# Optimization experiments

Measured on AMD Instinct MI355X. Metric: run time of the kernel, lower is better.

The kernel has to match this reference:

```python
import jax, jax.numpy as jnp
import numpy as np

BLOCK_SIZE = 64
WINDOW_SIZE = 256  # local_window pattern: each query block attends to blocks within the window
NEG_INF = -1e30


def setup_inputs() -> dict:
    key = jax.random.key(0)
    kq, kk, kv = jax.random.split(key, 3)
    B, S, H, D = 2, 4096, 16, 64
    q = jax.random.normal(kq, (B, S, H, D), dtype=jnp.float32)
    k = jax.random.normal(kk, (B, S, H, D), dtype=jnp.float32)
    v = jax.random.normal(kv, (B, S, H, D), dtype=jnp.float32)
    return {"q": q, "k": k, "v": v}


def _block_sparse_attn(q, k, v):
    # q, k, v: [B, S, H, D]
    B, S, H, D = q.shape
    bs = BLOCK_SIZE
    N = S // bs                      # number of blocks
    W = WINDOW_SIZE // bs            # window in blocks (4)
    half = W // 2
    offsets = jnp.arange(-half, half + 1)          # [K] neighbor offsets, K = W+1 = 5
    K = offsets.shape[0]

    i = jnp.arange(N)
    j = i[:, None] + offsets[None, :]              # [N, K] neighbor block ids
    valid = (j >= 0) & (j < N)                     # boundary mask
    jc = jnp.clip(j, 0, N - 1)

    # reshape into blocks: [B, H, N, bs, D]
    qb = q.reshape(B, N, bs, H, D).transpose(0, 3, 1, 2, 4)
    kb = k.reshape(B, N, bs, H, D).transpose(0, 3, 1, 2, 4)
    vb = v.reshape(B, N, bs, H, D).transpose(0, 3, 1, 2, 4)

    # gather only the active (neighbor) key/value blocks: [B, H, N, K, bs, D]
    kn = kb[:, :, jc]
    vn = vb[:, :, jc]

    scale = 1.0 / jnp.sqrt(jnp.asarray(D, dtype=q.dtype))
    # block scores: [B, H, N, bs, K, bs]
    scores = jnp.einsum('bhnqd,bhnkcd->bhnqkc', qb, kn) * scale
    scores = jnp.where(valid[None, None, :, None, :, None], scores, NEG_INF)

    # softmax over the union of active key blocks for each query block
    scores = scores.reshape(B, H, N, bs, K * bs)
    attn = jax.nn.softmax(scores, axis=-1)
    out = jnp.einsum('bhnqe,bhned->bhnqd', attn, vn.reshape(B, H, N, K * bs, D))

    # back to [B, S, H, D]
    return out.transpose(0, 2, 3, 1, 4).reshape(B, S, H, D)


def reference(q, k, v):
    return _block_sparse_attn(q, k, v)
```

## Files before the change

kernel.cpp:

```cpp
#include <hip/hip_runtime.h>

#define S_DIM 4096
#define H_DIM 16
#define D_DIM 64
#define N_BLK 64
#define NEG_INF_F (-1e30f)
#define QSCALE 0.125f

typedef __attribute__((ext_vector_type(4))) float f32x4;
typedef __attribute__((ext_vector_type(8))) short s16x8;
typedef __attribute__((ext_vector_type(4))) unsigned int u32x4;
typedef __attribute__((ext_vector_type(2))) unsigned int u32x2;

__device__ __forceinline__ unsigned int fbits(float f) {
    return __builtin_bit_cast(unsigned int, f);
}
__device__ __forceinline__ unsigned int pkbf(float a, float b) {
    return __builtin_amdgcn_perm(fbits(b) + 0x8000u, fbits(a) + 0x8000u, 0x07060302u);
}

__global__ __launch_bounds__(256, 2) void bsattn_kernel(
    const float* __restrict__ qg, const float* __restrict__ kg,
    const float* __restrict__ vg, float* __restrict__ outg)
{
    __shared__ unsigned int lds_vt[D_DIM * 256];

    const int tid  = threadIdx.x;
    const int w    = tid >> 6;
    const int lane = tid & 63;
    const int quad = lane >> 4;
    const int l16  = lane & 15;

    const int b  = blockIdx.z;
    const int h  = blockIdx.y;
    const int n0 = blockIdx.x << 2;
    const int n  = n0 + w;

    s16x8 bq[4][2];
#pragma unroll
    for (int qt = 0; qt < 4; ++qt) {
        const size_t qrow = ((size_t)(b * S_DIM + n * 64 + qt * 16 + l16) * H_DIM + h) * D_DIM;
#pragma unroll
        for (int hh = 0; hh < 2; ++hh) {
            const float4* qp = reinterpret_cast<const float4*>(qg + qrow + hh * 32 + quad * 8);
            float4 f0 = qp[0];
            float4 f1 = qp[1];
            u32x4 u;
            u.x = pkbf(f0.x * QSCALE, f0.y * QSCALE);
            u.y = pkbf(f0.z * QSCALE, f0.w * QSCALE);
            u.z = pkbf(f1.x * QSCALE, f1.y * QSCALE);
            u.w = pkbf(f1.z * QSCALE, f1.w * QSCALE);
            bq[qt][hh] = __builtin_bit_cast(s16x8, u);
        }
    }

    {
        const int jt = tid >> 5;
        const int sp = tid & 31;
        const int jv = n0 - 2 + jt;
        if (jv >= 0 && jv < N_BLK) {
            const float* v0p = vg + ((size_t)(b * S_DIM + jv * 64 + 2 * sp) * H_DIM + h) * D_DIM;
            const float* v1p = v0p + H_DIM * D_DIM;
            const int craw = jt * 64 + 2 * sp;
#pragma unroll
            for (int ch = 0; ch < 4; ++ch) {
                const int d0 = ch * 16;
                const float4* ap = reinterpret_cast<const float4*>(v0p + d0);
                const float4* bp = reinterpret_cast<const float4*>(v1p + d0);
                float4 a0 = ap[0], a1 = ap[1], a2 = ap[2], a3 = ap[3];
                float4 b0 = bp[0], b1 = bp[1], b2 = bp[2], b3 = bp[3];
                float av[16] = {a0.x,a0.y,a0.z,a0.w, a1.x,a1.y,a1.z,a1.w,
                                a2.x,a2.y,a2.z,a2.w, a3.x,a3.y,a3.z,a3.w};
                float bv[16] = {b0.x,b0.y,b0.z,b0.w, b1.x,b1.y,b1.z,b1.w,
                                b2.x,b2.y,b2.z,b2.w, b3.x,b3.y,b3.z,b3.w};
#pragma unroll
                for (int i = 0; i < 16; ++i) {
                    const int d = d0 + i;
                    lds_vt[d * 256 + (((craw + 8 * d) & 511) >> 1)] = pkbf(av[i], bv[i]);
                }
            }
        }
    }

    f32x4 o[4][4];
    float m_run[4], l_run[4];
#pragma unroll
    for (int qt = 0; qt < 4; ++qt) {
        m_run[qt] = NEG_INF_F; l_run[qt] = 0.f;
#pragma unroll
        for (int dt = 0; dt < 4; ++dt) o[qt][dt] = (f32x4){0.f, 0.f, 0.f, 0.f};
    }

    __syncthreads();

    const int colb = quad * 4 + 8 * l16;

    for (int t = 0; t < 5; ++t) {
        const int j = n - 2 + t;
        if (j < 0 || j >= N_BLK) continue;
        const int ji = w + t;

        float4 kf[4][2][2];
#pragma unroll
        for (int kt = 0; kt < 4; ++kt) {
            const size_t krow = ((size_t)(b * S_DIM + j * 64 + kt * 16 + l16) * H_DIM + h) * D_DIM + quad * 8;
#pragma unroll
            for (int hh = 0; hh < 2; ++hh) {
                const float4* kp = reinterpret_cast<const float4*>(kg + krow + hh * 32);
                kf[kt][hh][0] = kp[0];
                kf[kt][hh][1] = kp[1];
            }
        }
        s16x8 kbf[4][2];
#pragma unroll
        for (int kt = 0; kt < 4; ++kt)
#pragma unroll
            for (int hh = 0; hh < 2; ++hh) {
                u32x4 u;
                u.x = pkbf(kf[kt][hh][0].x, kf[kt][hh][0].y);
                u.y = pkbf(kf[kt][hh][0].z, kf[kt][hh][0].w);
                u.z = pkbf(kf[kt][hh][1].x, kf[kt][hh][1].y);
                u.w = pkbf(kf[kt][hh][1].z, kf[kt][hh][1].w);
                kbf[kt][hh] = __builtin_bit_cast(s16x8, u);
            }

        s16x8 pa[4][2];
#pragma unroll
        for (int qt = 0; qt < 4; ++qt) {
            f32x4 sa[4];
#pragma unroll
            for (int kt = 0; kt < 4; ++kt) {
                f32x4 z = {0.f, 0.f, 0.f, 0.f};
                f32x4 a0 = __builtin_amdgcn_mfma_f32_16x16x32_bf16(kbf[kt][0], bq[qt][0], z, 0, 0, 0);
                sa[kt]   = __builtin_amdgcn_mfma_f32_16x16x32_bf16(kbf[kt][1], bq[qt][1], a0, 0, 0, 0);
            }
            float mx = NEG_INF_F;
#pragma unroll
            for (int kt = 0; kt < 4; ++kt)
#pragma unroll
                for (int r = 0; r < 4; ++r) mx = fmaxf(mx, sa[kt][r]);
            mx = fmaxf(mx, __shfl_xor(mx, 16));
            mx = fmaxf(mx, __shfl_xor(mx, 32));
            const float mn = fmaxf(m_run[qt], mx);
            const float alpha = __expf(m_run[qt] - mn);
            m_run[qt] = mn;

            float rs = 0.f;
            unsigned int pk[4][2];
#pragma unroll
            for (int kt = 0; kt < 4; ++kt) {
                float e0 = __expf(sa[kt][0] - mn);
                float e1 = __expf(sa[kt][1] - mn);
                float e2 = __expf(sa[kt][2] - mn);
                float e3 = __expf(sa[kt][3] - mn);
                rs += (e0 + e1) + (e2 + e3);
                pk[kt][0] = pkbf(e0, e1);
                pk[kt][1] = pkbf(e2, e3);
            }
            rs += __shfl_xor(rs, 16);
            rs += __shfl_xor(rs, 32);
            l_run[qt] = l_run[qt] * alpha + rs;

            float ab[4];
#pragma unroll
            for (int r = 0; r < 4; ++r)
                ab[r] = __shfl(alpha, (lane & 48) + quad * 4 + r);
#pragma unroll
            for (int dt = 0; dt < 4; ++dt)
#pragma unroll
                for (int r = 0; r < 4; ++r) o[qt][dt][r] *= ab[r];

            pa[qt][0] = __builtin_bit_cast(s16x8, (u32x4){pk[0][0], pk[0][1], pk[1][0], pk[1][1]});
            pa[qt][1] = __builtin_bit_cast(s16x8, (u32x4){pk[2][0], pk[2][1], pk[3][0], pk[3][1]});
        }

        const int cb0 = ji * 64 + colb;
#pragma unroll
        for (int dt = 0; dt < 4; ++dt) {
            const int d = dt * 16 + l16;
            const unsigned int* vrow = lds_vt + d * 256;
            const int cb = cb0 + 128 * dt;
            u32x2 v00 = *reinterpret_cast<const u32x2*>(vrow + (((cb     ) & 511) >> 1));
            u32x2 v01 = *reinterpret_cast<const u32x2*>(vrow + (((cb + 16) & 511) >> 1));
            u32x2 v10 = *reinterpret_cast<const u32x2*>(vrow + (((cb + 32) & 511) >> 1));
            u32x2 v11 = *reinterpret_cast<const u32x2*>(vrow + (((cb + 48) & 511) >> 1));
            s16x8 vf0 = __builtin_bit_cast(s16x8, (u32x4){v00.x, v00.y, v01.x, v01.y});
            s16x8 vf1 = __builtin_bit_cast(s16x8, (u32x4){v10.x, v10.y, v11.x, v11.y});
#pragma unroll
            for (int qt = 0; qt < 4; ++qt) {
                o[qt][dt] = __builtin_amdgcn_mfma_f32_16x16x32_bf16(pa[qt][0], vf0, o[qt][dt], 0, 0, 0);
                o[qt][dt] = __builtin_amdgcn_mfma_f32_16x16x32_bf16(pa[qt][1], vf1, o[qt][dt], 0, 0, 0);
            }
        }
    }

#pragma unroll
    for (int qt = 0; qt < 4; ++qt) {
#pragma unroll
        for (int r = 0; r < 4; ++r) {
            const float lb = __shfl(l_run[qt], (lane & 48) + quad * 4 + r);
            const float inv = 1.0f / lb;
            const int row = n * 64 + qt * 16 + quad * 4 + r;
            float* op = outg + ((size_t)(b * S_DIM + row) * H_DIM + h) * D_DIM + l16;
#pragma unroll
            for (int dt = 0; dt < 4; ++dt)
                op[dt * 16] = o[qt][dt][r] * inv;
        }
    }
}

extern "C" void kernel_launch(void* const* d_in, const int* in_sizes, int n_in,
                              void* d_out, int out_size, void* d_ws, size_t ws_size,
                              hipStream_t stream) {
    const float* q = (const float*)d_in[0];
    const float* k = (const float*)d_in[1];
    const float* v = (const float*)d_in[2];
    float* out = (float*)d_out;
    const int B = in_sizes[0] / (S_DIM * H_DIM * D_DIM);
    dim3 grid(N_BLK / 4, H_DIM, B);
    dim3 block(256);
    hipLaunchKernelGGL(bsattn_kernel, grid, block, 0, stream, q, k, v, out);
}
```

Measured before the change: 159.7 us.

## Software-pipeline K block loads with double-buffered registers across window tiles

Unrolls the five-tile window loop and prefetches the next K block into a second register buffer while the current tile's QK, softmax and PV MFMAs run. Clamped block indices keep the loads in bounds, and boundary tiles skip only the compute. This targets global-load latency that was exposed at the start of each tile. The extra registers lead to lowering launch bounds from two blocks per CU to one, which can reduce occupancy and latency hiding across waves.

After: 173.3 us. +8.5%, slower.

```diff
diff --git a/kernel.cpp b/kernel.cpp
--- a/kernel.cpp
+++ b/kernel.cpp
@@ -19,7 +19,109 @@
     return __builtin_amdgcn_perm(fbits(b) + 0x8000u, fbits(a) + 0x8000u, 0x07060302u);
 }
 
-__global__ __launch_bounds__(256, 2) void bsattn_kernel(
+__device__ __forceinline__ void load_k(const float* __restrict__ kb, float4 (&kf)[4][2][2]) {
+#pragma unroll
+    for (int kt = 0; kt < 4; ++kt) {
+        const float4* kp = reinterpret_cast<const float4*>(kb + (size_t)kt * (16 * H_DIM * D_DIM));
+#pragma unroll
+        for (int hh = 0; hh < 2; ++hh) {
+            kf[kt][hh][0] = kp[hh * 8 + 0];
+            kf[kt][hh][1] = kp[hh * 8 + 1];
+        }
+    }
+}
+
+__device__ __forceinline__ void conv_k(const float4 (&kf)[4][2][2], s16x8 (&kbf)[4][2]) {
+#pragma unroll
+    for (int kt = 0; kt < 4; ++kt)
+#pragma unroll
+        for (int hh = 0; hh < 2; ++hh) {
+            u32x4 u;
+            u.x = pkbf(kf[kt][hh][0].x, kf[kt][hh][0].y);
+            u.y = pkbf(kf[kt][hh][0].z, kf[kt][hh][0].w);
+            u.z = pkbf(kf[kt][hh][1].x, kf[kt][hh][1].y);
+            u.w = pkbf(kf[kt][hh][1].z, kf[kt][hh][1].w);
+            kbf[kt][hh] = __builtin_bit_cast(s16x8, u);
+        }
+}
+
+__device__ __forceinline__ void compute_tile(
+    const s16x8 (&kbf)[4][2], const s16x8 (&bq)[4][2],
+    f32x4 (&o)[4][4], float (&m_run)[4], float (&l_run)[4],
+    const unsigned int* __restrict__ lds_vt, int cb0, int lane, int quad)
+{
+    s16x8 pa[4][2];
+#pragma unroll
+    for (int qt = 0; qt < 4; ++qt) {
+        f32x4 sa[4];
+#pragma unroll
+        for (int kt = 0; kt < 4; ++kt) {
+            f32x4 z = {0.f, 0.f, 0.f, 0.f};
+            f32x4 a0 = __builtin_amdgcn_mfma_f32_16x16x32_bf16(kbf[kt][0], bq[qt][0], z, 0, 0, 0);
+            sa[kt]   = __builtin_amdgcn_mfma_f32_16x16x32_bf16(kbf[kt][1], bq[qt][1], a0, 0, 0, 0);
+        }
+        const float ma = fmaxf(fmaxf(sa[0][0], sa[0][1]), fmaxf(sa[0][2], sa[0][3]));
+        const float mb = fmaxf(fmaxf(sa[1][0], sa[1][1]), fmaxf(sa[1][2], sa[1][3]));
+        const float mc = fmaxf(fmaxf(sa[2][0], sa[2][1]), fmaxf(sa[2][2], sa[2][3]));
+        const float md = fmaxf(fmaxf(sa[3][0], sa[3][1]), fmaxf(sa[3][2], sa[3][3]));
+        float mx = fmaxf(fmaxf(ma, mb), fmaxf(mc, md));
+        mx = fmaxf(mx, __shfl_xor(mx, 16));
+        mx = fmaxf(mx, __shfl_xor(mx, 32));
+        const float mn = fmaxf(m_run[qt], mx);
+        const float alpha = __expf(m_run[qt] - mn);
+        m_run[qt] = mn;
+
+        float rsk[4];
+        unsigned int pk[4][2];
+#pragma unroll
+        for (int kt = 0; kt < 4; ++kt) {
+            float e0 = __expf(sa[kt][0] - mn);
+            float e1 = __expf(sa[kt][1] - mn);
+            float e2 = __expf(sa[kt][2] - mn);
+            float e3 = __expf(sa[kt][3] - mn);
+            rsk[kt] = (e0 + e1) + (e2 + e3);
+            pk[kt][0] = pkbf(e0, e1);
+            pk[kt][1] = pkbf(e2, e3);
+        }
+        float rs = (rsk[0] + rsk[1]) + (rsk[2] + rsk[3]);
+        rs += __shfl_xor(rs, 16);
+        rs += __shfl_xor(rs, 32);
+        l_run[qt] = l_run[qt] * alpha + rs;
+
+        float ab[4];
+#pragma unroll
+        for (int r = 0; r < 4; ++r)
+            ab[r] = __shfl(alpha, (lane & 48) + quad * 4 + r);
+#pragma unroll
+        for (int dt = 0; dt < 4; ++dt)
+#pragma unroll
+            for (int r = 0; r < 4; ++r) o[qt][dt][r] *= ab[r];
+
+        pa[qt][0] = __builtin_bit_cast(s16x8, (u32x4){pk[0][0], pk[0][1], pk[1][0], pk[1][1]});
+        pa[qt][1] = __builtin_bit_cast(s16x8, (u32x4){pk[2][0], pk[2][1], pk[3][0], pk[3][1]});
+    }
+
+    const int l16 = lane & 15;
+#pragma unroll
+    for (int dt = 0; dt < 4; ++dt) {
+        const int d = dt * 16 + l16;
+        const unsigned int* vrow = lds_vt + d * 256;
+        const int cb = cb0 + 128 * dt;
+        u32x2 v00 = *reinterpret_cast<const u32x2*>(vrow + (((cb     ) & 511) >> 1));
+        u32x2 v01 = *reinterpret_cast<const u32x2*>(vrow + (((cb + 16) & 511) >> 1));
+        u32x2 v10 = *reinterpret_cast<const u32x2*>(vrow + (((cb + 32) & 511) >> 1));
+        u32x2 v11 = *reinterpret_cast<const u32x2*>(vrow + (((cb + 48) & 511) >> 1));
+        s16x8 vf0 = __builtin_bit_cast(s16x8, (u32x4){v00.x, v00.y, v01.x, v01.y});
+        s16x8 vf1 = __builtin_bit_cast(s16x8, (u32x4){v10.x, v10.y, v11.x, v11.y});
+#pragma unroll
+        for (int qt = 0; qt < 4; ++qt) {
+            o[qt][dt] = __builtin_amdgcn_mfma_f32_16x16x32_bf16(pa[qt][0], vf0, o[qt][dt], 0, 0, 0);
+            o[qt][dt] = __builtin_amdgcn_mfma_f32_16x16x32_bf16(pa[qt][1], vf1, o[qt][dt], 0, 0, 0);
+        }
+    }
+}
+
+__global__ __launch_bounds__(256, 1) void bsattn_kernel(
     const float* __restrict__ qg, const float* __restrict__ kg,
     const float* __restrict__ vg, float* __restrict__ outg)
 {
@@ -35,6 +137,14 @@
     const int h  = blockIdx.y;
     const int n0 = blockIdx.x << 2;
     const int n  = n0 + w;
+
+    const float* kbase = kg + ((size_t)(b * S_DIM) * H_DIM + h) * D_DIM + ((size_t)l16 * H_DIM) * D_DIM + quad * 8;
+#define KPTR(jj) (kbase + (size_t)(jj) * (64 * H_DIM * D_DIM))
+#define JCLAMP(jj) ((jj) < 0 ? 0 : ((jj) > (N_BLK - 1) ? (N_BLK - 1) : (jj)))
+
+    float4 kfA[4][2][2], kfB[4][2][2];
+    s16x8 kbf[4][2];
+    load_k(KPTR(JCLAMP(n - 2)), kfA);
 
     s16x8 bq[4][2];
 #pragma unroll
@@ -95,104 +205,32 @@
 
     const int colb = quad * 4 + 8 * l16;
 
-    for (int t = 0; t < 5; ++t) {
-        const int j = n - 2 + t;
-        if (j < 0 || j >= N_BLK) continue;
-        const int ji = w + t;
-
-        float4 kf[4][2][2];
-#pragma unroll
-        for (int kt = 0; kt < 4; ++kt) {
-            const size_t krow = ((size_t)(b * S_DIM + j * 64 + kt * 16 + l16) * H_DIM + h) * D_DIM + quad * 8;
-#pragma unroll
-            for (int hh = 0; hh < 2; ++hh) {
-                const float4* kp = reinterpret_cast<const float4*>(kg + krow + hh * 32);
-                kf[kt][hh][0] = kp[0];
-                kf[kt][hh][1] = kp[1];
-            }
-        }
-        s16x8 kbf[4][2];
-#pragma unroll
-        for (int kt = 0; kt < 4; ++kt)
-#pragma unroll
-            for (int hh = 0; hh < 2; ++hh) {
-                u32x4 u;
-                u.x = pkbf(kf[kt][hh][0].x, kf[kt][hh][0].y);
-                u.y = pkbf(kf[kt][hh][0].z, kf[kt][hh][0].w);
-                u.z = pkbf(kf[kt][hh][1].x, kf[kt][hh][1].y);
-                u.w = pkbf(kf[kt][hh][1].z, kf[kt][hh][1].w);
-                kbf[kt][hh] = __builtin_bit_cast(s16x8, u);
-            }
-
-        s16x8 pa[4][2];
-#pragma unroll
-        for (int qt = 0; qt < 4; ++qt) {
-            f32x4 sa[4];
-#pragma unroll
-            for (int kt = 0; kt < 4; ++kt) {
-                f32x4 z = {0.f, 0.f, 0.f, 0.f};
-                f32x4 a0 = __builtin_amdgcn_mfma_f32_16x16x32_bf16(kbf[kt][0], bq[qt][0], z, 0, 0, 0);
-                sa[kt]   = __builtin_amdgcn_mfma_f32_16x16x32_bf16(kbf[kt][1], bq[qt][1], a0, 0, 0, 0);
-            }
-            float mx = NEG_INF_F;
-#pragma unroll
-            for (int kt = 0; kt < 4; ++kt)
-#pragma unroll
-                for (int r = 0; r < 4; ++r) mx = fmaxf(mx, sa[kt][r]);
-            mx = fmaxf(mx, __shfl_xor(mx, 16));
-            mx = fmaxf(mx, __shfl_xor(mx, 32));
-            const float mn = fmaxf(m_run[qt], mx);
-            const float alpha = __expf(m_run[qt] - mn);
-            m_run[qt] = mn;
-
-            float rs = 0.f;
-            unsigned int pk[4][2];
-#pragma unroll
-            for (int kt = 0; kt < 4; ++kt) {
-                float e0 = __expf(sa[kt][0] - mn);
-                float e1 = __expf(sa[kt][1] - mn);
-                float e2 = __expf(sa[kt][2] - mn);
-                float e3 = __expf(sa[kt][3] - mn);
-                rs += (e0 + e1) + (e2 + e3);
-                pk[kt][0] = pkbf(e0, e1);
-                pk[kt][1] = pkbf(e2, e3);
-            }
-            rs += __shfl_xor(rs, 16);
-            rs += __shfl_xor(rs, 32);
-            l_run[qt] = l_run[qt] * alpha + rs;
-
-            float ab[4];
-#pragma unroll
-            for (int r = 0; r < 4; ++r)
-                ab[r] = __shfl(alpha, (lane & 48) + quad * 4 + r);
-#pragma unroll
-            for (int dt = 0; dt < 4; ++dt)
-#pragma unroll
-                for (int r = 0; r < 4; ++r) o[qt][dt][r] *= ab[r];
-
-            pa[qt][0] = __builtin_bit_cast(s16x8, (u32x4){pk[0][0], pk[0][1], pk[1][0], pk[1][1]});
-            pa[qt][1] = __builtin_bit_cast(s16x8, (u32x4){pk[2][0], pk[2][1], pk[3][0], pk[3][1]});
-        }
-
-        const int cb0 = ji * 64 + colb;
-#pragma unroll
-        for (int dt = 0; dt < 4; ++dt) {
-            const int d = dt * 16 + l16;
-            const unsigned int* vrow = lds_vt + d * 256;
-            const int cb = cb0 + 128 * dt;
-            u32x2 v00 = *reinterpret_cast<const u32x2*>(vrow + (((cb     ) & 511) >> 1));
-            u32x2 v01 = *reinterpret_cast<const u32x2*>(vrow + (((cb + 16) & 511) >> 1));
-            u32x2 v10 = *reinterpret_cast<const u32x2*>(vrow + (((cb + 32) & 511) >> 1));
-            u32x2 v11 = *reinterpret_cast<const u32x2*>(vrow + (((cb + 48) & 511) >> 1));
-            s16x8 vf0 = __builtin_bit_cast(s16x8, (u32x4){v00.x, v00.y, v01.x, v01.y});
-            s16x8 vf1 = __builtin_bit_cast(s16x8, (u32x4){v10.x, v10.y, v11.x, v11.y});
-#pragma unroll
-            for (int qt = 0; qt < 4; ++qt) {
-                o[qt][dt] = __builtin_amdgcn_mfma_f32_16x16x32_bf16(pa[qt][0], vf0, o[qt][dt], 0, 0, 0);
-                o[qt][dt] = __builtin_amdgcn_mfma_f32_16x16x32_bf16(pa[qt][1], vf1, o[qt][dt], 0, 0, 0);
-            }
-        }
-    }
+    conv_k(kfA, kbf);
+
+    load_k(KPTR(JCLAMP(n - 1)), kfB);
+    if (n - 2 >= 0)
+        compute_tile(kbf, bq, o, m_run, l_run, lds_vt, (w + 0) * 64 + colb, lane, quad);
+    conv_k(kfB, kbf);
+
+    load_k(KPTR(JCLAMP(n)), kfA);
+    if (n - 1 >= 0)
+        compute_tile(kbf, bq, o, m_run, l_run, lds_vt, (w + 1) * 64 + colb, lane, quad);
+    conv_k(kfA, kbf);
+
+    load_k(KPTR(JCLAMP(n + 1)), kfB);
+    compute_tile(kbf, bq, o, m_run, l_run, lds_vt, (w + 2) * 64 + colb, lane, quad);
+    conv_k(kfB, kbf);
+
+    load_k(KPTR(JCLAMP(n + 2)), kfA);
+    if (n + 1 < N_BLK)
+        compute_tile(kbf, bq, o, m_run, l_run, lds_vt, (w + 3) * 64 + colb, lane, quad);
+    conv_k(kfA, kbf);
+
+    if (n + 2 < N_BLK)
+        compute_tile(kbf, bq, o, m_run, l_run, lds_vt, (w + 4) * 64 + colb, lane, quad);
+
+#undef KPTR
+#undef JCLAMP
 
 #pragma unroll
     for (int qt = 0; qt < 4; ++qt) {
```

## Stage shared K blocks in LDS as bf16 fragments across warps

Applied to the files above, without the earlier changes.

Each workgroup now loads the 8 neighboring K blocks once, converts them to bf16 and stores them in LDS already laid out as MFMA fragments. Each warp then reads its fragments from LDS instead of reloading K from global memory and repacking it per tile. This cuts redundant global K traffic, since the four warps previously fetched overlapping blocks, and removes repeated conversion work. In exchange LDS use grows by 64KB per workgroup and launch bounds drop to one workgroup per SIMD group, which lowers occupancy and latency hiding.

Result: slower. 167.4 us (+4.9%).

```diff
diff --git a/kernel.cpp b/kernel.cpp
--- a/kernel.cpp
+++ b/kernel.cpp
@@ -19,11 +19,88 @@
     return __builtin_amdgcn_perm(fbits(b) + 0x8000u, fbits(a) + 0x8000u, 0x07060302u);
 }
 
-__global__ __launch_bounds__(256, 2) void bsattn_kernel(
+__device__ __forceinline__ void compute_tile(
+    const s16x8 (&kbf)[4][2], const s16x8 (&bq)[4][2],
+    f32x4 (&o)[4][4], float (&m_run)[4], float (&l_run)[4],
+    const unsigned int* __restrict__ lds_vt, int cb0, int lane, int quad)
+{
+    s16x8 pa[4][2];
+#pragma unroll
+    for (int qt = 0; qt < 4; ++qt) {
+        f32x4 sa[4];
+#pragma unroll
+        for (int kt = 0; kt < 4; ++kt) {
+            f32x4 z = {0.f, 0.f, 0.f, 0.f};
+            f32x4 a0 = __builtin_amdgcn_mfma_f32_16x16x32_bf16(kbf[kt][0], bq[qt][0], z, 0, 0, 0);
+            sa[kt]   = __builtin_amdgcn_mfma_f32_16x16x32_bf16(kbf[kt][1], bq[qt][1], a0, 0, 0, 0);
+        }
+        const float ma = fmaxf(fmaxf(sa[0][0], sa[0][1]), fmaxf(sa[0][2], sa[0][3]));
+        const float mb = fmaxf(fmaxf(sa[1][0], sa[1][1]), fmaxf(sa[1][2], sa[1][3]));
+        const float mc = fmaxf(fmaxf(sa[2][0], sa[2][1]), fmaxf(sa[2][2], sa[2][3]));
+        const float md = fmaxf(fmaxf(sa[3][0], sa[3][1]), fmaxf(sa[3][2], sa[3][3]));
+        float mx = fmaxf(fmaxf(ma, mb), fmaxf(mc, md));
+        mx = fmaxf(mx, __shfl_xor(mx, 16));
+        mx = fmaxf(mx, __shfl_xor(mx, 32));
+        const float mn = fmaxf(m_run[qt], mx);
+        const float alpha = __expf(m_run[qt] - mn);
+        m_run[qt] = mn;
+
+        float rsk[4];
+        unsigned int pk[4][2];
+#pragma unroll
+        for (int kt = 0; kt < 4; ++kt) {
+            float e0 = __expf(sa[kt][0] - mn);
+            float e1 = __expf(sa[kt][1] - mn);
+            float e2 = __expf(sa[kt][2] - mn);
+            float e3 = __expf(sa[kt][3] - mn);
+            rsk[kt] = (e0 + e1) + (e2 + e3);
+            pk[kt][0] = pkbf(e0, e1);
+            pk[kt][1] = pkbf(e2, e3);
+        }
+        float rs = (rsk[0] + rsk[1]) + (rsk[2] + rsk[3]);
+        rs += __shfl_xor(rs, 16);
+        rs += __shfl_xor(rs, 32);
+        l_run[qt] = l_run[qt] * alpha + rs;
+
+        float ab[4];
+#pragma unroll
+        for (int r = 0; r < 4; ++r)
+            ab[r] = __shfl(alpha, (lane & 48) + quad * 4 + r);
+#pragma unroll
+        for (int dt = 0; dt < 4; ++dt)
+#pragma unroll
+            for (int r = 0; r < 4; ++r) o[qt][dt][r] *= ab[r];
+
+        pa[qt][0] = __builtin_bit_cast(s16x8, (u32x4){pk[0][0], pk[0][1], pk[1][0], pk[1][1]});
+        pa[qt][1] = __builtin_bit_cast(s16x8, (u32x4){pk[2][0], pk[2][1], pk[3][0], pk[3][1]});
+    }
+
+    const int l16 = lane & 15;
+#pragma unroll
+    for (int dt = 0; dt < 4; ++dt) {
+        const int d = dt * 16 + l16;
+        const unsigned int* vrow = lds_vt + d * 256;
+        const int cb = cb0 + 128 * dt;
+        u32x2 v00 = *reinterpret_cast<const u32x2*>(vrow + (((cb     ) & 511) >> 1));
+        u32x2 v01 = *reinterpret_cast<const u32x2*>(vrow + (((cb + 16) & 511) >> 1));
+        u32x2 v10 = *reinterpret_cast<const u32x2*>(vrow + (((cb + 32) & 511) >> 1));
+        u32x2 v11 = *reinterpret_cast<const u32x2*>(vrow + (((cb + 48) & 511) >> 1));
+        s16x8 vf0 = __builtin_bit_cast(s16x8, (u32x4){v00.x, v00.y, v01.x, v01.y});
+        s16x8 vf1 = __builtin_bit_cast(s16x8, (u32x4){v10.x, v10.y, v11.x, v11.y});
+#pragma unroll
+        for (int qt = 0; qt < 4; ++qt) {
+            o[qt][dt] = __builtin_amdgcn_mfma_f32_16x16x32_bf16(pa[qt][0], vf0, o[qt][dt], 0, 0, 0);
+            o[qt][dt] = __builtin_amdgcn_mfma_f32_16x16x32_bf16(pa[qt][1], vf1, o[qt][dt], 0, 0, 0);
+        }
+    }
+}
+
+__global__ __launch_bounds__(256, 1) void bsattn_kernel(
     const float* __restrict__ qg, const float* __restrict__ kg,
     const float* __restrict__ vg, float* __restrict__ outg)
 {
     __shared__ unsigned int lds_vt[D_DIM * 256];
+    __shared__ unsigned int lds_kf[8 * 2048];
 
     const int tid  = threadIdx.x;
     const int w    = tid >> 6;
@@ -54,6 +131,26 @@
         }
     }
 
+#pragma unroll
+    for (int jt = 0; jt < 8; ++jt) {
+        const int jv = n0 - 2 + jt;
+        if (jv < 0 || jv >= N_BLK) continue;
+#pragma unroll
+        for (int s = 0; s < 2; ++s) {
+            const int slot = s * 256 + tid;
+            const int key  = slot >> 3;
+            const int dc   = slot & 7;
+            const float* kp = kg + ((size_t)(b * S_DIM + jv * 64 + key) * H_DIM + h) * D_DIM + dc * 8;
+            const float4 f0 = reinterpret_cast<const float4*>(kp)[0];
+            const float4 f1 = reinterpret_cast<const float4*>(kp)[1];
+            const u32x4 u = {pkbf(f0.x, f0.y), pkbf(f0.z, f0.w),
+                             pkbf(f1.x, f1.y), pkbf(f1.z, f1.w)};
+            const int lanew = (key & 15) + 16 * (dc & 3);
+            const int fidx  = ((key >> 4) << 1) + (dc >> 2);
+            *reinterpret_cast<u32x4*>(lds_kf + jt * 2048 + (fidx * 64 + lanew) * 4) = u;
+        }
+    }
+
     {
         const int jt = tid >> 5;
         const int sp = tid & 31;
@@ -100,98 +197,16 @@
         if (j < 0 || j >= N_BLK) continue;
         const int ji = w + t;
 
-        float4 kf[4][2][2];
-#pragma unroll
-        for (int kt = 0; kt < 4; ++kt) {
-            const size_t krow = ((size_t)(b * S_DIM + j * 64 + kt * 16 + l16) * H_DIM + h) * D_DIM + quad * 8;
-#pragma unroll
-            for (int hh = 0; hh < 2; ++hh) {
-                const float4* kp = reinterpret_cast<const float4*>(kg + krow + hh * 32);
-                kf[kt][hh][0] = kp[0];
-                kf[kt][hh][1] = kp[1];
-            }
-        }
+        const unsigned int* kfp = lds_kf + ji * 2048 + lane * 4;
         s16x8 kbf[4][2];
 #pragma unroll
         for (int kt = 0; kt < 4; ++kt)
 #pragma unroll
-            for (int hh = 0; hh < 2; ++hh) {
-                u32x4 u;
-                u.x = pkbf(kf[kt][hh][0].x, kf[kt][hh][0].y);
-                u.y = pkbf(kf[kt][hh][0].z, kf[kt][hh][0].w);
-                u.z = pkbf(kf[kt][hh][1].x, kf[kt][hh][1].y);
-                u.w = pkbf(kf[kt][hh][1].z, kf[kt][hh][1].w);
-                kbf[kt][hh] = __builtin_bit_cast(s16x8, u);
-            }
-
-        s16x8 pa[4][2];
-#pragma unroll
-        for (int qt = 0; qt < 4; ++qt) {
-            f32x4 sa[4];
-#pragma unroll
-            for (int kt = 0; kt < 4; ++kt) {
-                f32x4 z = {0.f, 0.f, 0.f, 0.f};
-                f32x4 a0 = __builtin_amdgcn_mfma_f32_16x16x32_bf16(kbf[kt][0], bq[qt][0], z, 0, 0, 0);
-                sa[kt]   = __builtin_amdgcn_mfma_f32_16x16x32_bf16(kbf[kt][1], bq[qt][1], a0, 0, 0, 0);
-            }
-            float mx = NEG_INF_F;
-#pragma unroll
-            for (int kt = 0; kt < 4; ++kt)
-#pragma unroll
-                for (int r = 0; r < 4; ++r) mx = fmaxf(mx, sa[kt][r]);
-            mx = fmaxf(mx, __shfl_xor(mx, 16));
-            mx = fmaxf(mx, __shfl_xor(mx, 32));
-            const float mn = fmaxf(m_run[qt], mx);
-            const float alpha = __expf(m_run[qt] - mn);
-            m_run[qt] = mn;
-
-            float rs = 0.f;
-            unsigned int pk[4][2];
-#pragma unroll
-            for (int kt = 0; kt < 4; ++kt) {
-                float e0 = __expf(sa[kt][0] - mn);
-                float e1 = __expf(sa[kt][1] - mn);
-                float e2 = __expf(sa[kt][2] - mn);
-                float e3 = __expf(sa[kt][3] - mn);
-                rs += (e0 + e1) + (e2 + e3);
-                pk[kt][0] = pkbf(e0, e1);
-                pk[kt][1] = pkbf(e2, e3);
-            }
-            rs += __shfl_xor(rs, 16);
-            rs += __shfl_xor(rs, 32);
-            l_run[qt] = l_run[qt] * alpha + rs;
-
-            float ab[4];
-#pragma unroll
-            for (int r = 0; r < 4; ++r)
-                ab[r] = __shfl(alpha, (lane & 48) + quad * 4 + r);
-#pragma unroll
-            for (int dt = 0; dt < 4; ++dt)
-#pragma unroll
-                for (int r = 0; r < 4; ++r) o[qt][dt][r] *= ab[r];
-
-            pa[qt][0] = __builtin_bit_cast(s16x8, (u32x4){pk[0][0], pk[0][1], pk[1][0], pk[1][1]});
-            pa[qt][1] = __builtin_bit_cast(s16x8, (u32x4){pk[2][0], pk[2][1], pk[3][0], pk[3][1]});
-        }
-
-        const int cb0 = ji * 64 + colb;
-#pragma unroll
-        for (int dt = 0; dt < 4; ++dt) {
-            const int d = dt * 16 + l16;
-            const unsigned int* vrow = lds_vt + d * 256;
-            const int cb = cb0 + 128 * dt;
-            u32x2 v00 = *reinterpret_cast<const u32x2*>(vrow + (((cb     ) & 511) >> 1));
-            u32x2 v01 = *reinterpret_cast<const u32x2*>(vrow + (((cb + 16) & 511) >> 1));
-            u32x2 v10 = *reinterpret_cast<const u32x2*>(vrow + (((cb + 32) & 511) >> 1));
-            u32x2 v11 = *reinterpret_cast<const u32x2*>(vrow + (((cb + 48) & 511) >> 1));
-            s16x8 vf0 = __builtin_bit_cast(s16x8, (u32x4){v00.x, v00.y, v01.x, v01.y});
-            s16x8 vf1 = __builtin_bit_cast(s16x8, (u32x4){v10.x, v10.y, v11.x, v11.y});
-#pragma unroll
-            for (int qt = 0; qt < 4; ++qt) {
-                o[qt][dt] = __builtin_amdgcn_mfma_f32_16x16x32_bf16(pa[qt][0], vf0, o[qt][dt], 0, 0, 0);
-                o[qt][dt] = __builtin_amdgcn_mfma_f32_16x16x32_bf16(pa[qt][1], vf1, o[qt][dt], 0, 0, 0);
-            }
-        }
+            for (int hh = 0; hh < 2; ++hh)
+                kbf[kt][hh] = __builtin_bit_cast(s16x8,
+                    *reinterpret_cast<const u32x4*>(kfp + ((kt << 1) + hh) * 256));
+
+        compute_tile(kbf, bq, o, m_run, l_run, lds_vt, ji * 64 + colb, lane, quad);
     }
 
 #pragma unroll
```
